# Optimization experiments

Measured on AMD Instinct MI355X. Metric: run time of the kernel, lower is better.

## Reference

```python
import jax, jax.numpy as jnp
import numpy as np

DIM = 2048
N_HEADS = 32
N_KV_HEADS = 8
HEAD_DIM = DIM // N_HEADS  # 64
N_REP = N_HEADS // N_KV_HEADS  # 4
B, S = 2, 2048
MASK_VAL = -32768.0


def setup_inputs() -> dict:
    key = jax.random.key(0)
    ks = jax.random.split(key, 7)
    x = jax.random.normal(ks[0], (B, S, DIM), dtype=jnp.float32)
    freqs_cos = jax.random.uniform(ks[1], (S, HEAD_DIM // 2), dtype=jnp.float32)
    freqs_sin = jax.random.uniform(ks[2], (S, HEAD_DIM // 2), dtype=jnp.float32)
    sc = 1.0 / np.sqrt(DIM)
    wq = jax.random.normal(ks[3], (N_HEADS * HEAD_DIM, DIM), dtype=jnp.float32) * sc
    wk = jax.random.normal(ks[4], (N_KV_HEADS * HEAD_DIM, DIM), dtype=jnp.float32) * sc
    wv = jax.random.normal(ks[5], (N_KV_HEADS * HEAD_DIM, DIM), dtype=jnp.float32) * sc
    wo = jax.random.normal(ks[6], (DIM, N_HEADS * HEAD_DIM), dtype=jnp.float32) * sc
    return {"x": x, "freqs_cos": freqs_cos, "freqs_sin": freqs_sin,
            "wq": wq, "wk": wk, "wv": wv, "wo": wo}


def _apply_rope(q, k, cos, sin):
    # q: [B,S,H,D], k: [B,S,Hkv,D]; interleaved real/imag pairs in last dim
    def rot(t):
        tr = t.reshape(t.shape[:-1] + (-1, 2))  # [..., D/2, 2]
        t_r, t_i = tr[..., 0], tr[..., 1]
        c = cos[None, :, None, :]  # broadcast over batch and heads
        s = sin[None, :, None, :]
        o_r = t_r * c - t_i * s
        o_i = t_r * s + t_i * c
        return jnp.stack([o_r, o_i], axis=-1).reshape(t.shape)
    return rot(q), rot(k)


def reference(x, freqs_cos, freqs_sin, wq, wk, wv, wo):
    bsz, seqlen, _ = x.shape
    xq = (x @ wq.T).reshape(bsz, seqlen, N_HEADS, HEAD_DIM)
    xk = (x @ wk.T).reshape(bsz, seqlen, N_KV_HEADS, HEAD_DIM)
    xv = (x @ wv.T).reshape(bsz, seqlen, N_KV_HEADS, HEAD_DIM)
    xq, xk = _apply_rope(xq, xk, freqs_cos, freqs_sin)
    # GQA: repeat each kv head n_rep times contiguously (matches per-head cat loop)
    xk = jnp.repeat(xk, N_REP, axis=2)  # [B,S,H,D]
    xv = jnp.repeat(xv, N_REP, axis=2)
    # [B,H,S,D]
    q = xq.transpose(0, 2, 1, 3)
    k = xk.transpose(0, 2, 1, 3)
    v = xv.transpose(0, 2, 1, 3)
    scores = jnp.einsum('bhqd,bhkd->bhqk', q, k) / jnp.sqrt(jnp.float32(HEAD_DIM))
    causal = jnp.triu(jnp.full((seqlen, seqlen), MASK_VAL, dtype=scores.dtype), k=1)
    scores = scores + causal[None, None, :, :]
    probs = jax.nn.softmax(scores.astype(jnp.float32), axis=-1).astype(q.dtype)
    out = jnp.einsum('bhqk,bhkd->bhqd', probs, v)
    out = out.transpose(0, 2, 1, 3).reshape(bsz, seqlen, -1)
    return out @ wo.T
```

## Files before the change

kernel.cpp:

```cpp
#include <hip/hip_runtime.h>
#include <hip/hip_bf16.h>
#include <type_traits>

typedef __bf16 bf16;
typedef __bf16 bf16x2 __attribute__((ext_vector_type(2)));
typedef __bf16 bf16x4 __attribute__((ext_vector_type(4)));
typedef __bf16 bf16x8 __attribute__((ext_vector_type(8)));
typedef float f32x4 __attribute__((ext_vector_type(4)));

#define AS1 __attribute__((address_space(1)))
#define AS3 __attribute__((address_space(3)))

#define KAPPA 0.180336880111f

__device__ __forceinline__ void load_lds16(const void* g, void* l) {
  __builtin_amdgcn_global_load_lds((AS1 void*)g, (AS3 void*)l, 16, 0, 0);
}
__device__ __forceinline__ float exp2_fast(float x) {
  return __builtin_amdgcn_exp2f(x);
}

__global__ void f2b_all(const float* __restrict__ x, const float* __restrict__ wq,
                        const float* __restrict__ wk, const float* __restrict__ wv,
                        const float* __restrict__ wo, bf16* __restrict__ xb,
                        bf16* __restrict__ wqkv, bf16* __restrict__ wob) {
  int bid = blockIdx.x;
  if (bid < 8192) {
    int i = (bid * 256 + threadIdx.x) * 4;
    float4 v = *(const float4*)(x + i);
    bf16x4 o = {(bf16)v.x, (bf16)v.y, (bf16)v.z, (bf16)v.w};
    *(bf16x4*)(xb + i) = o;
    return;
  }
  const float* src;
  bf16* dst;
  int off;
  if (bid < 10240) { src = wq; dst = wqkv; off = bid - 8192; }
  else if (bid < 10752) { src = wk; dst = wqkv + 4194304; off = bid - 10240; }
  else if (bid < 11264) { src = wv; dst = wqkv + 5242880; off = bid - 10752; }
  else { src = wo; dst = wob; off = bid - 11264; }
  int i = (off * 256 + threadIdx.x) * 8;
  int n = i >> 11, k = i & 2047;
  float4 v0 = *(const float4*)(src + (size_t)n * 2048 + k);
  float4 v1 = *(const float4*)(src + (size_t)n * 2048 + k + 4);
  bf16x8 o = {(bf16)v0.x, (bf16)v0.y, (bf16)v0.z, (bf16)v0.w,
              (bf16)v1.x, (bf16)v1.y, (bf16)v1.z, (bf16)v1.w};
  size_t dstb = ((size_t)((n >> 6) * 64 + (k >> 5))) * 4096 +
                (size_t)((n >> 4) & 3) * 1024 +
                (size_t)((n & 15) | (((k >> 3) & 3) << 4)) * 16;
  *(bf16x8*)((char*)dst + dstb) = o;
}

__global__ __launch_bounds__(256, 3) void gemm_qkv(const bf16* __restrict__ A,
                                                   const bf16* __restrict__ Bw,
                                                   const float* __restrict__ fc,
                                                   const float* __restrict__ fs,
                                                   bf16* __restrict__ Qro,
                                                   bf16* __restrict__ Kro,
                                                   bf16* __restrict__ Vt) {
  const int K = 2048;
  __shared__ bf16 As[3][128][32];
  const int t = threadIdx.x;
  const int wave = t >> 6, lane = t & 63, qd = lane >> 4, ln = lane & 15;
  const int wm = (wave >> 1) * 64;
  const int wn = (wave & 1) * 64;
  const int bn = blockIdx.x;
  const size_t bm = (size_t)blockIdx.y * 128;

  const bf16* Ab = A + bm * (size_t)K;
  const int n0 = bn * 2 + (wn >> 6);
  const char* Bb = (const char*)Bw + (size_t)n0 * 262144 + (size_t)lane * 16;

  auto stage = [&](int tk, int slot) {
#pragma unroll
    for (int sub = 0; sub < 2; sub++) {
      int e = sub * 256 + t;
      int ro = e >> 2, gs = (e & 3) ^ ((ro >> 1) & 3);
      load_lds16(Ab + (size_t)ro * K + tk * 32 + gs * 8,
                 (char*)As + slot * 8192 + sub * 4096 + wave * 1024);
    }
  };

  f32x4 acc[4][4] = {};
  const int segoff = (qd ^ ((ln >> 1) & 3)) << 4;
  bf16x8 b0[4], b1[4];

#pragma unroll
  for (int j = 0; j < 4; j++)
    b0[j] = *(const bf16x8*)(Bb + (size_t)j * 1024);
  stage(0, 0);
  stage(1, 1);
  asm volatile("s_waitcnt vmcnt(2)" ::: "memory");
  __builtin_amdgcn_s_barrier();

  auto step = [&](int tk, bf16x8 (&cb)[4], bf16x8 (&nb)[4]) {
    if (tk < 62) stage(tk + 2, (tk + 2) % 3);
    if (tk < 63) {
#pragma unroll
      for (int j = 0; j < 4; j++)
        nb[j] = *(const bf16x8*)(Bb + (size_t)(tk + 1) * 4096 + j * 1024);
    }
    const char* Asl = (const char*)As + (tk % 3) * 8192;
    bf16x8 af[4];
#pragma unroll
    for (int i = 0; i < 4; i++)
      af[i] = *(const bf16x8*)(Asl + (wm + i * 16 + ln) * 64 + segoff);
    if (tk <= 61) asm volatile("s_waitcnt lgkmcnt(0) vmcnt(6)" ::: "memory");
    else if (tk == 62) asm volatile("s_waitcnt lgkmcnt(0) vmcnt(4)" ::: "memory");
    else asm volatile("s_waitcnt lgkmcnt(0) vmcnt(0)" ::: "memory");
    __builtin_amdgcn_sched_barrier(0);
    __builtin_amdgcn_s_setprio(1);
#pragma unroll
    for (int i = 0; i < 4; i++)
#pragma unroll
      for (int j = 0; j < 4; j++)
        acc[i][j] = __builtin_amdgcn_mfma_f32_16x16x32_bf16(af[i], cb[j],
                                                            acc[i][j], 0, 0, 0);
    __builtin_amdgcn_s_setprio(0);
    if (tk < 63) __builtin_amdgcn_s_barrier();
  };

  for (int tk = 0; tk < 64; tk += 2) {
    step(tk, b0, b1);
    step(tk + 1, b1, b0);
  }

  const int b = (int)(bm >> 11);
  const int sb = (int)(bm & 2047) + wm;
  const bool odd = ln & 1;

  if (bn < 20) {
    const bool isQ = bn < 16;
    const float kap = isQ ? KAPPA : 1.0f;
    const int hh = isQ ? (bn * 2 + (wn >> 6)) : ((bn - 16) * 2 + (wn >> 6));
    bf16* dst = isQ ? (Qro + ((size_t)(b * 32 + hh) * 2048) * 64)
                    : (Kro + ((size_t)(b * 8 + hh) * 2048) * 64);
#pragma unroll
    for (int i = 0; i < 4; i++) {
#pragma unroll
      for (int j = 0; j < 4; j++) {
        const int d = j * 16 + ln;
        const int i_f = d >> 1;
#pragma unroll
        for (int r = 0; r < 4; r++) {
          int s = sb + i * 16 + qd * 4 + r;
          float v = acc[i][j][r];
          float p = __shfl_xor(v, 1);
          float cv = fc[s * 32 + i_f] * kap;
          float sv = fs[s * 32 + i_f] * kap;
          float o = odd ? (p * sv + v * cv) : (v * cv - p * sv);
          dst[(size_t)s * 64 + d] = (bf16)o;
        }
      }
    }
  } else {
    const int kh = (bn - 20) * 2 + (wn >> 6);
#pragma unroll
    for (int i = 0; i < 4; i++)
#pragma unroll
      for (int j = 0; j < 4; j++) {
        const int d = j * 16 + ln;
        int s = sb + i * 16 + qd * 4;
        bf16x4 ov = {(bf16)acc[i][j][0], (bf16)acc[i][j][1],
                     (bf16)acc[i][j][2], (bf16)acc[i][j][3]};
        *(bf16x4*)&Vt[((size_t)(b * 8 + kh) * 64 + d) * 2048 + s] = ov;
      }
  }
}

__global__ __launch_bounds__(256, 2) void gemm_bt(const bf16* __restrict__ A,
                                                  const bf16* __restrict__ Bw,
                                                  float* __restrict__ C) {
  const int K = 2048, N = 2048;
  __shared__ bf16 As[3][128][32];
  const int t = threadIdx.x;
  const int wave = t >> 6, lane = t & 63, qd = lane >> 4, ln = lane & 15;
  const int wm = (wave >> 1) * 64;
  const int wn = (wave & 1) * 64;
  const size_t bm = (size_t)blockIdx.y * 128;
  const size_t bn = (size_t)blockIdx.x * 128;

  const bf16* Ab = A + bm * (size_t)K;
  const int n0 = (int)(bn >> 6) + (wn >> 6);
  const char* Bb = (const char*)Bw + (size_t)n0 * 262144 + (size_t)lane * 16;

  auto stage = [&](int tk, int slot) {
#pragma unroll
    for (int sub = 0; sub < 2; sub++) {
      int e = sub * 256 + t;
      int ro = e >> 2, gs = (e & 3) ^ ((ro >> 1) & 3);
      load_lds16(Ab + (size_t)ro * K + tk * 32 + gs * 8,
                 (char*)As + slot * 8192 + sub * 4096 + wave * 1024);
    }
  };

  f32x4 acc[4][4] = {};
  const int segoff = (qd ^ ((ln >> 1) & 3)) << 4;
  bf16x8 b0[4], b1[4];

#pragma unroll
  for (int j = 0; j < 4; j++)
    b0[j] = *(const bf16x8*)(Bb + (size_t)j * 1024);
  stage(0, 0);
  stage(1, 1);
  asm volatile("s_waitcnt vmcnt(2)" ::: "memory");
  __builtin_amdgcn_s_barrier();

  auto step = [&](int tk, bf16x8 (&cb)[4], bf16x8 (&nb)[4]) {
    if (tk < 62) stage(tk + 2, (tk + 2) % 3);
    if (tk < 63) {
#pragma unroll
      for (int j = 0; j < 4; j++)
        nb[j] = *(const bf16x8*)(Bb + (size_t)(tk + 1) * 4096 + j * 1024);
    }
    const char* Asl = (const char*)As + (tk % 3) * 8192;
    bf16x8 af[4];
#pragma unroll
    for (int i = 0; i < 4; i++)
      af[i] = *(const bf16x8*)(Asl + (wm + i * 16 + ln) * 64 + segoff);
    if (tk <= 61) asm volatile("s_waitcnt lgkmcnt(0) vmcnt(6)" ::: "memory");
    else if (tk == 62) asm volatile("s_waitcnt lgkmcnt(0) vmcnt(4)" ::: "memory");
    else asm volatile("s_waitcnt lgkmcnt(0) vmcnt(0)" ::: "memory");
    __builtin_amdgcn_sched_barrier(0);
    __builtin_amdgcn_s_setprio(1);
#pragma unroll
    for (int i = 0; i < 4; i++)
#pragma unroll
      for (int j = 0; j < 4; j++)
        acc[i][j] = __builtin_amdgcn_mfma_f32_16x16x32_bf16(af[i], cb[j],
                                                            acc[i][j], 0, 0, 0);
    __builtin_amdgcn_s_setprio(0);
    if (tk < 63) __builtin_amdgcn_s_barrier();
  };

  for (int tk = 0; tk < 64; tk += 2) {
    step(tk, b0, b1);
    step(tk + 1, b1, b0);
  }

#pragma unroll
  for (int i = 0; i < 4; i++)
#pragma unroll
    for (int j = 0; j < 4; j++)
#pragma unroll
      for (int r = 0; r < 4; r++) {
        size_t row = bm + wm + i * 16 + qd * 4 + r;
        size_t col = bn + wn + j * 16 + ln;
        C[row * N + col] = acc[i][j][r];
      }
}

__global__ __launch_bounds__(256, 3) void attn_fwd(const bf16* __restrict__ Q,
                                                   const bf16* __restrict__ Kg,
                                                   const bf16* __restrict__ Vg,
                                                   bf16* __restrict__ O) {
  __shared__ bf16 Ks[2][64][64];
  __shared__ bf16 Vs[2][64][64];
  __shared__ bf16 Ps[128][64];
  const int t = threadIdx.x;
  const int wave = t >> 6, lane = t & 63, qd = lane >> 4, ln = lane & 15;
  const int bid = blockIdx.x;
  const int qt = 15 - (bid >> 6);
  const int bh = bid & 63;
  const int b = bh >> 5, h = bh & 31, kh = h >> 2;
  const bf16* Qb = Q + ((size_t)(b * 32 + h) * 2048 + qt * 128) * 64;
  const bf16* Kb = Kg + (size_t)(b * 8 + kh) * 2048 * 64;
  const bf16* Vb = Vg + (size_t)(b * 8 + kh) * 64 * 2048;
  char* PsB = (char*)Ps;

  bf16x8 qf[2][2];
#pragma unroll
  for (int kk = 0; kk < 2; kk++)
#pragma unroll
    for (int mi = 0; mi < 2; mi++)
      qf[kk][mi] = *(const bf16x8*)(Qb + (wave * 32 + mi * 16 + ln) * 64 +
                                    (kk * 4 + qd) * 8);

  auto stageKV = [&](int kb, int buf) {
#pragma unroll
    for (int i = 0; i < 2; i++) {
      int e = i * 256 + t;
      int row = e >> 3, sg = (e & 7) ^ (row & 7);
      load_lds16(Kb + (size_t)(kb * 64 + row) * 64 + sg * 8,
                 (char*)Ks + buf * 8192 + i * 4096 + wave * 1024);
      load_lds16(Vb + (size_t)row * 2048 + kb * 64 + sg * 8,
                 (char*)Vs + buf * 8192 + i * 4096 + wave * 1024);
    }
  };

  f32x4 o_acc[4][2] = {};
  float l_st[2] = {0.f, 0.f};
  const int q0 = qt * 128 + wave * 32;
  const int nkb = 2 * qt + 2;

  stageKV(0, 0);
  __syncthreads();

  for (int kb = 0; kb < nkb; kb++) {
    const int cur = kb & 1;
    if (kb + 1 < nkb) stageKV(kb + 1, cur ^ 1);
    const char* Ksl = (const char*)Ks + cur * 8192;
    const char* Vsl = (const char*)Vs + cur * 8192;

    f32x4 s_acc[4][2] = {};
#pragma unroll
    for (int kk = 0; kk < 2; kk++) {
      bf16x8 ak[4];
#pragma unroll
      for (int j = 0; j < 4; j++) {
        int row = j * 16 + ln;
        int ph = (kk * 4 + qd) ^ (ln & 7);
        ak[j] = *(const bf16x8*)(Ksl + row * 128 + ph * 16);
      }
#pragma unroll
      for (int j = 0; j < 4; j++)
#pragma unroll
        for (int mi = 0; mi < 2; mi++)
          s_acc[j][mi] = __builtin_amdgcn_mfma_f32_16x16x32_bf16(
              ak[j], qf[kk][mi], s_acc[j][mi], 0, 0, 0);
    }

    auto smax = [&](auto maskc) {
      constexpr bool MASK = decltype(maskc)::value;
#pragma unroll
      for (int mi = 0; mi < 2; mi++) {
        const int qv = q0 + mi * 16 + ln;
        const int prow = wave * 32 + mi * 16 + ln;
        float rs = 0.f;
#pragma unroll
        for (int j = 0; j < 4; j++) {
          bf16x4 pk;
#pragma unroll
          for (int r = 0; r < 4; r++) {
            float s = s_acc[j][mi][r];
            if (MASK) {
              int k_glob = kb * 64 + j * 16 + qd * 4 + r;
              if (k_glob > qv) s = -1e5f;
            }
            float pv = exp2_fast(s - 16.f);
            rs += pv;
            pk[r] = (bf16)pv;
          }
          int ps = (j * 2 + (qd >> 1)) ^ (ln & 7);
          *(bf16x4*)(PsB + prow * 128 + ps * 16 + (qd & 1) * 8) = pk;
        }
        l_st[mi] += rs;
      }
    };
    if (kb * 64 + 63 > q0) smax(std::true_type{});
    else smax(std::false_type{});

#pragma unroll
    for (int kk = 0; kk < 2; kk++) {
      bf16x8 av[4], bp[2];
#pragma unroll
      for (int dj = 0; dj < 4; dj++) {
        int row = dj * 16 + ln;
        int ph = (kk * 4 + qd) ^ (ln & 7);
        av[dj] = *(const bf16x8*)(Vsl + row * 128 + ph * 16);
      }
#pragma unroll
      for (int mi = 0; mi < 2; mi++) {
        int prow = wave * 32 + mi * 16 + ln;
        int ph = (kk * 4 + qd) ^ (ln & 7);
        bp[mi] = *(const bf16x8*)(PsB + prow * 128 + ph * 16);
      }
#pragma unroll
      for (int dj = 0; dj < 4; dj++)
#pragma unroll
        for (int mi = 0; mi < 2; mi++)
          o_acc[dj][mi] = __builtin_amdgcn_mfma_f32_16x16x32_bf16(
              av[dj], bp[mi], o_acc[dj][mi], 0, 0, 0);
    }

    __syncthreads();
  }

#pragma unroll
  for (int mi = 0; mi < 2; mi++) {
    float lt = l_st[mi];
    lt += __shfl_xor(lt, 16);
    lt += __shfl_xor(lt, 32);
    float inv = 1.f / lt;
    int q_idx = qt * 128 + wave * 32 + mi * 16 + ln;
#pragma unroll
    for (int dj = 0; dj < 4; dj++) {
      bf16x4 ov;
#pragma unroll
      for (int r = 0; r < 4; r++) ov[r] = (bf16)(o_acc[dj][mi][r] * inv);
      *(bf16x4*)&O[((size_t)(b * 2048 + q_idx) * 32 + h) * 64 + dj * 16 + qd * 4] = ov;
    }
  }
}

extern "C" void kernel_launch(void* const* d_in, const int* in_sizes, int n_in,
                              void* d_out, int out_size, void* d_ws,
                              size_t ws_size, hipStream_t stream) {
  const float* x = (const float*)d_in[0];
  const float* fc = (const float*)d_in[1];
  const float* fs = (const float*)d_in[2];
  const float* wq = (const float*)d_in[3];
  const float* wk = (const float*)d_in[4];
  const float* wv = (const float*)d_in[5];
  const float* wo = (const float*)d_in[6];
  float* out = (float*)d_out;

  char* ws = (char*)d_ws;
  const size_t MB = (size_t)1 << 20;
  bf16* xb   = (bf16*)(ws + 0 * MB);
  bf16* wqkv = (bf16*)(ws + 16 * MB);
  bf16* wob  = (bf16*)(ws + 28 * MB);
  bf16* Qro  = (bf16*)(ws + 36 * MB);
  bf16* Kro  = (bf16*)(ws + 52 * MB);
  bf16* Vt   = (bf16*)(ws + 56 * MB);
  bf16* Oa   = (bf16*)(ws + 60 * MB);

  dim3 blk(256);
  f2b_all<<<13312, blk, 0, stream>>>(x, wq, wk, wv, wo, xb, wqkv, wob);
  gemm_qkv<<<dim3(24, 32), blk, 0, stream>>>(xb, wqkv, fc, fs, Qro, Kro, Vt);
  attn_fwd<<<1024, blk, 0, stream>>>(Qro, Kro, Vt, Oa);
  gemm_bt<<<dim3(16, 32), blk, 0, stream>>>(Oa, wob, out);
}
```

Measured before the change: 291.2 us.

## Remap workgroup indices for XCD-aware L2 locality in GEMMs and attention

Flattens the GEMM grids to 1D and remaps block IDs so that blocks landing on the same XCD (round-robin by wg&7) share B-column tiles and A-row panels, improving L2 reuse. Attention also remaps its (batch, head) index so that consecutive blocks on one XCD work on heads sharing the same KV head. The weight conversion kernel now assigns each block one 64x32 tile, so its global reads are tile-shaped and its writes are contiguous, with the same destination layout as before. The cost is slightly more index arithmetic, and the benefit depends on how the hardware dispatches blocks to XCDs.

New measurement: 271.9 us. 1.07x faster.

```diff
diff --git a/kernel.cpp b/kernel.cpp
--- a/kernel.cpp
+++ b/kernel.cpp
@@ -32,23 +32,35 @@
     *(bf16x4*)(xb + i) = o;
     return;
   }
+  int bid2 = bid - 8192;
   const float* src;
   bf16* dst;
-  int off;
-  if (bid < 10240) { src = wq; dst = wqkv; off = bid - 8192; }
-  else if (bid < 10752) { src = wk; dst = wqkv + 4194304; off = bid - 10240; }
-  else if (bid < 11264) { src = wv; dst = wqkv + 5242880; off = bid - 10752; }
-  else { src = wo; dst = wob; off = bid - 11264; }
-  int i = (off * 256 + threadIdx.x) * 8;
-  int n = i >> 11, k = i & 2047;
+  int nblk, kblk, nb;
+  if (bid2 < 3072) {
+    nblk = bid2 >> 6;
+    kblk = bid2 & 63;
+    int n0 = nblk * 64;
+    if (n0 < 2048) { src = wq; nb = n0; }
+    else if (n0 < 2560) { src = wk; nb = n0 - 2048; }
+    else { src = wv; nb = n0 - 2560; }
+    dst = wqkv;
+  } else {
+    int bid3 = bid2 - 3072;
+    nblk = bid3 >> 6;
+    kblk = bid3 & 63;
+    src = wo;
+    nb = nblk * 64;
+    dst = wob;
+  }
+  const int t = threadIdx.x, j = t >> 6, l = t & 63;
+  const int n = nb + j * 16 + (l & 15);
+  const int k = kblk * 32 + (l >> 4) * 8;
   float4 v0 = *(const float4*)(src + (size_t)n * 2048 + k);
   float4 v1 = *(const float4*)(src + (size_t)n * 2048 + k + 4);
   bf16x8 o = {(bf16)v0.x, (bf16)v0.y, (bf16)v0.z, (bf16)v0.w,
               (bf16)v1.x, (bf16)v1.y, (bf16)v1.z, (bf16)v1.w};
-  size_t dstb = ((size_t)((n >> 6) * 64 + (k >> 5))) * 4096 +
-                (size_t)((n >> 4) & 3) * 1024 +
-                (size_t)((n & 15) | (((k >> 3) & 3) << 4)) * 16;
-  *(bf16x8*)((char*)dst + dstb) = o;
+  *(bf16x8*)((char*)dst + ((size_t)(nblk * 64 + kblk)) * 4096 + j * 1024 +
+             l * 16) = o;
 }
 
 __global__ __launch_bounds__(256, 3) void gemm_qkv(const bf16* __restrict__ A,
@@ -64,8 +76,10 @@
   const int wave = t >> 6, lane = t & 63, qd = lane >> 4, ln = lane & 15;
   const int wm = (wave >> 1) * 64;
   const int wn = (wave & 1) * 64;
-  const int bn = blockIdx.x;
-  const size_t bm = (size_t)blockIdx.y * 128;
+  const int wg = blockIdx.x;
+  const int swz = (wg & 7) * 96 + (wg >> 3);
+  const int bn = swz >> 5;
+  const size_t bm = (size_t)(swz & 31) * 128;
 
   const bf16* Ab = A + bm * (size_t)K;
   const int n0 = bn * 2 + (wn >> 6);
@@ -177,8 +191,10 @@
   const int wave = t >> 6, lane = t & 63, qd = lane >> 4, ln = lane & 15;
   const int wm = (wave >> 1) * 64;
   const int wn = (wave & 1) * 64;
-  const size_t bm = (size_t)blockIdx.y * 128;
-  const size_t bn = (size_t)blockIdx.x * 128;
+  const int wg = blockIdx.x;
+  const int swz = (wg & 7) * 64 + (wg >> 3);
+  const size_t bn = (size_t)(swz >> 5) * 128;
+  const size_t bm = (size_t)(swz & 31) * 128;
 
   const bf16* Ab = A + bm * (size_t)K;
   const int n0 = (int)(bn >> 6) + (wn >> 6);
@@ -261,7 +277,8 @@
   const int wave = t >> 6, lane = t & 63, qd = lane >> 4, ln = lane & 15;
   const int bid = blockIdx.x;
   const int qt = 15 - (bid >> 6);
-  const int bh = bid & 63;
+  const int r0 = bid & 63;
+  const int bh = (r0 & 7) * 8 + (r0 >> 3);
   const int b = bh >> 5, h = bh & 31, kh = h >> 2;
   const bf16* Qb = Q + ((size_t)(b * 32 + h) * 2048 + qt * 128) * 64;
   const bf16* Kb = Kg + (size_t)(b * 8 + kh) * 2048 * 64;
@@ -417,7 +434,7 @@
 
   dim3 blk(256);
   f2b_all<<<13312, blk, 0, stream>>>(x, wq, wk, wv, wo, xb, wqkv, wob);
-  gemm_qkv<<<dim3(24, 32), blk, 0, stream>>>(xb, wqkv, fc, fs, Qro, Kro, Vt);
+  gemm_qkv<<<768, blk, 0, stream>>>(xb, wqkv, fc, fs, Qro, Kro, Vt);
   attn_fwd<<<1024, blk, 0, stream>>>(Qro, Kro, Vt, Oa);
-  gemm_bt<<<dim3(16, 32), blk, 0, stream>>>(Oa, wob, out);
-}
+  gemm_bt<<<512, blk, 0, stream>>>(Oa, wob, out);
+}
```
